# Kernel optimization log

Hardware: AMD Instinct MI355X
Metric: run time of the kernel (lower is better)

## Reference

```python
import jax, jax.numpy as jnp
import numpy as np

TWO_PI = 2.0 * np.pi
B, S_IN, S_OUT, K, HID = 1024, 4096, 4096, 8, 512
EPS = 1e-6


def setup_inputs() -> dict:
    key = jax.random.key(0)
    k1, k2, k3, k4, k5, k6, k7, k8 = jax.random.split(key, 8)
    x_in = jax.random.uniform(k1, (B, S_OUT), dtype=jnp.float32) * TWO_PI
    x_passive = jax.random.normal(k2, (B, S_IN), dtype=jnp.float32)
    log_density = jax.random.normal(k3, (B, 1), dtype=jnp.float32)
    # MLP params (nn.Linear default-ish init scale)
    lim1 = 1.0 / np.sqrt(S_IN)
    lim2 = 1.0 / np.sqrt(HID)
    w1 = jax.random.uniform(k4, (S_IN, HID), jnp.float32, -lim1, lim1)
    b1 = jax.random.uniform(k5, (HID,), jnp.float32, -lim1, lim1)
    w2 = jax.random.uniform(k6, (HID, S_OUT * 3 * K), jnp.float32, -lim2, lim2)
    b2 = jax.random.uniform(k7, (S_OUT * 3 * K,), jnp.float32, -lim2, lim2)
    phase_shift = jax.random.uniform(k8, (1,), jnp.float32)
    return {"x_in": x_in, "x_passive": x_passive, "log_density": log_density,
            "w1": w1, "b1": b1, "w2": w2, "b2": b2, "phase_shift": phase_shift}


def reference(x_in, x_passive, log_density, w1, b1, w2, b2, phase_shift):
    # normalise network input with global mean / (unbiased) std, as torch does
    xn = (x_passive - x_passive.mean()) / x_passive.std(ddof=1)
    # dense network: Linear -> tanh -> Linear -> tanh (final_activation=activation)
    net = jnp.tanh(jnp.tanh(xn @ w1 + b1) @ w2 + b2)            # (B, S*3K)
    net = net.reshape(-1, S_OUT, 3 * K)
    h_raw, w_raw, d_raw = net[..., :K], net[..., K:2 * K], net[..., 2 * K:]
    h_norm = jax.nn.softmax(h_raw, axis=2) * TWO_PI              # (B,S,K)
    w_norm = jax.nn.softmax(w_raw, axis=2) * TWO_PI
    d_norm = jax.nn.softplus(d_raw)
    bshape = (h_norm.shape[0], S_OUT, 1)
    x_kp = jnp.concatenate([jnp.full(bshape, -EPS, h_norm.dtype),
                            jnp.cumsum(w_norm, axis=2)], axis=2)  # (B,S,K+1)
    phi_kp = jnp.concatenate([jnp.zeros(bshape, h_norm.dtype),
                              jnp.cumsum(h_norm, axis=2)], axis=2)
    x = x_in[..., None]                                          # (B,S,1)
    # searchsorted (left) per element: count of knots strictly less than x, minus 1
    k_ind = jnp.sum(x_kp < x, axis=2, keepdims=True) - 1         # (B,S,1) int
    k_ind = jnp.clip(k_ind, 0, K - 1)
    g = lambda a, i: jnp.take_along_axis(a, i, axis=2)
    w_k = g(w_norm, k_ind)
    h_k = g(h_norm, k_ind)
    s_k = h_k / w_k
    d_k = g(d_norm, k_ind)
    d_kp1 = g(d_norm, (k_ind + 1) % K)
    x_km1 = g(x_kp, k_ind)
    phi_km1 = g(phi_kp, k_ind)
    alpha = (x - x_km1) / w_k
    a1m = alpha * (1.0 - alpha)
    denom = s_k + (d_kp1 + d_k - 2.0 * s_k) * a1m
    phi_out = (phi_km1 + h_k * (s_k * alpha ** 2 + d_k * a1m) / denom)[..., 0]
    phi_out = (phi_out + phase_shift) % TWO_PI                   # (B,S)
    grad = s_k ** 2 * (d_kp1 * alpha ** 2 + 2.0 * s_k * a1m
                       + d_k * (1.0 - alpha) ** 2) / denom ** 2  # (B,S,1)
    log_density = log_density - jnp.log(grad).sum(axis=1)        # (B,1)
    return phi_out, log_density
```

## Files before the change

kernel.cpp:

```cpp
#include <hip/hip_runtime.h>
#include <cstdint>
#include <cstddef>


typedef unsigned short u16;
typedef __bf16 bf16x8 __attribute__((ext_vector_type(8)));
typedef float f32x4 __attribute__((ext_vector_type(4)));
typedef unsigned short u16x8 __attribute__((ext_vector_type(8)));
typedef unsigned short u16x4 __attribute__((ext_vector_type(4)));
typedef unsigned short u16x2 __attribute__((ext_vector_type(2)));

#define TWOPI_F 6.28318530717958647692f

static __device__ __forceinline__ u16 f32_to_bf16(float f){
  unsigned u = __builtin_bit_cast(unsigned, f);
  return (u16)((u + 0x7fffu + ((u >> 16) & 1u)) >> 16);
}
static __device__ __forceinline__ void async16(void* lds, const void* g){
  __builtin_amdgcn_global_load_lds((const __attribute__((address_space(1))) void*)g,
                                   (__attribute__((address_space(3))) void*)lds,
                                   16, 0, 0);
}
static __device__ __forceinline__ float rcpf(float x){ return __builtin_amdgcn_rcpf(x); }
static __device__ __forceinline__ float fast_tanh(float x){
  x = fminf(fmaxf(x, -15.f), 15.f);
  float e = __expf(2.f * x);
  return (e - 1.f) / (e + 1.f);
}
static __device__ __forceinline__ float tanh_nc(float x){
  const float e2 = __expf(2.f * x);
  return 1.f - 2.f * rcpf(e2 + 1.f);
}
static __device__ __forceinline__ float exp_tanh(float x){
  const float e2 = __expf(2.f * x);
  const float u  = rcpf(e2 + 1.f);
  return __expf(1.f - 2.f * u);
}
static __device__ __forceinline__ float softplus_f(float x){
  return fmaxf(x, 0.f) + __logf(1.f + __expf(-fabsf(x)));
}

__global__ void k_stats(const float* __restrict__ xp, float* __restrict__ stats){
  __shared__ float ss[4], sq[4];
  const int tid = threadIdx.x;
  const long gt = (long)blockIdx.x * 256 + tid;
  const float4* x4 = (const float4*)xp;
  float s = 0.f, q = 0.f;
  #pragma unroll
  for (int p = 0; p < 4; ++p){
    float4 v = x4[gt + (long)p * 262144];
    s += v.x + v.y + v.z + v.w;
    q += v.x*v.x + v.y*v.y + v.z*v.z + v.w*v.w;
  }
  #pragma unroll
  for (int off = 32; off; off >>= 1){
    s += __shfl_down(s, off);
    q += __shfl_down(q, off);
  }
  if ((tid & 63) == 0){ ss[tid>>6] = s; sq[tid>>6] = q; }
  __syncthreads();
  if (tid == 0){
    atomicAdd(stats,     ss[0]+ss[1]+ss[2]+ss[3]);
    atomicAdd(stats + 1, sq[0]+sq[1]+sq[2]+sq[3]);
  }
}

__global__ void k_prep(const float* __restrict__ xp, const float* __restrict__ stats,
                       u16* __restrict__ xn){
  const long t = (long)blockIdx.x * 256 + threadIdx.x;
  const float sum = stats[0], sq = stats[1];
  const float N = 4194304.f;
  const float mean = sum / N;
  const float istd = rsqrtf((sq - sum*sum/N) / (N - 1.f));
  const float4* x4 = (const float4*)xp;
  const float4 a = x4[2*t], b = x4[2*t+1];
  u16x8 o;
  o[0]=f32_to_bf16((a.x-mean)*istd); o[1]=f32_to_bf16((a.y-mean)*istd);
  o[2]=f32_to_bf16((a.z-mean)*istd); o[3]=f32_to_bf16((a.w-mean)*istd);
  o[4]=f32_to_bf16((b.x-mean)*istd); o[5]=f32_to_bf16((b.y-mean)*istd);
  o[6]=f32_to_bf16((b.z-mean)*istd); o[7]=f32_to_bf16((b.w-mean)*istd);
  ((u16x8*)xn)[t] = o;
}

__global__ __launch_bounds__(256) void k_transpose_cvt(const float* __restrict__ in,
                                                       u16* __restrict__ out,
                                                       int Kd, int Nd){
  __shared__ __align__(16) u16 tT[128*256];
  const int tid = threadIdx.x;
  const long k0 = (long)blockIdx.x * 256, n0 = (long)blockIdx.y * 128;
  const int lam = tid & 31, g = tid >> 5;
  const int c = lam * 4;
  const int sig = (lam & 7) << 2;
  #pragma unroll
  for (int pass = 0; pass < 16; ++pass){
    const int P = pass*8 + g;
    const float4 f0 = *(const float4*)&in[(k0 + 2*P    )*Nd + n0 + c];
    const float4 f1 = *(const float4*)&in[(k0 + 2*P + 1)*Nd + n0 + c];
    const int pp = 2*(P ^ sig);
    *(u16x2*)&tT[(c    )*256 + pp] = u16x2{f32_to_bf16(f0.x), f32_to_bf16(f1.x)};
    *(u16x2*)&tT[(c + 1)*256 + pp] = u16x2{f32_to_bf16(f0.y), f32_to_bf16(f1.y)};
    *(u16x2*)&tT[(c + 2)*256 + pp] = u16x2{f32_to_bf16(f0.z), f32_to_bf16(f1.z)};
    *(u16x2*)&tT[(c + 3)*256 + pp] = u16x2{f32_to_bf16(f0.w), f32_to_bf16(f1.w)};
  }
  __syncthreads();
  const int w = tid >> 6, l = tid & 63;
  const int lh = l >> 5, lk = l & 31;
  #pragma unroll
  for (int it = 0; it < 16; ++it){
    const int n = (w << 5) + (it << 1) + lh;
    const int s2 = (n >> 2) & 7;
    const u16x8 v = *(const u16x8*)&tT[n*256 + 8*(lk ^ s2)];
    *(u16x8*)&out[(n0 + n)*Kd + k0 + 8*lk] = v;
  }
}

__global__ __launch_bounds__(256, 2) void k_gemm1(
    const u16* __restrict__ xn,
    const u16* __restrict__ w1t,
    float* __restrict__ pp)
{
  __shared__ __align__(16) u16 sA[4][64*32];
  __shared__ __align__(16) u16 sB[4][64*32];
  const int tid = threadIdx.x, lane = tid & 63, w = tid >> 6;
  const int n0 = blockIdx.x << 6, m0 = blockIdx.y << 6;
  const int ks = blockIdx.z;
  const int wm = w >> 1, wn = w & 1;
  const int rA = lane >> 2, cA = (lane & 3) << 3;
  const int fr = lane & 15, fq = lane >> 4;
  const f32x4 z4 = {0.f, 0.f, 0.f, 0.f};
  f32x4 acc[2][2];
  #pragma unroll
  for (int i=0;i<2;i++){ acc[i][0] = z4; acc[i][1] = z4; }

  auto stage = [&](int kt){
    const int b = kt & 3;
    const int kofs = (ks << 11) + (kt << 5) + cA;
    async16(sA[b] + w*512, xn  + (long)(m0 + w*16 + rA)*4096 + kofs);
    async16(sB[b] + w*512, w1t + (long)(n0 + w*16 + rA)*4096 + kofs);
  };

  stage(0); stage(1);
  for (int kt = 0; kt < 64; ++kt){
    if (kt < 62){
      stage(kt + 2);
      asm volatile("s_waitcnt vmcnt(4)" ::: "memory");
    } else if (kt == 62){
      asm volatile("s_waitcnt vmcnt(2)" ::: "memory");
    } else {
      asm volatile("s_waitcnt vmcnt(0)" ::: "memory");
    }
    __builtin_amdgcn_s_barrier();
    const int b = kt & 3;
    bf16x8 af[2], bfv[2];
    #pragma unroll
    for (int i=0;i<2;i++) af[i]  = *(const bf16x8*)(sA[b] + ((wm<<5) + i*16 + fr)*32 + (fq<<3));
    #pragma unroll
    for (int j=0;j<2;j++) bfv[j] = *(const bf16x8*)(sB[b] + ((wn<<5) + j*16 + fr)*32 + (fq<<3));
    #pragma unroll
    for (int i=0;i<2;i++)
      #pragma unroll
      for (int j=0;j<2;j++)
        acc[i][j] = __builtin_amdgcn_mfma_f32_16x16x32_bf16(af[i], bfv[j], acc[i][j], 0, 0, 0);
  }
  float* po = pp + ((size_t)ks << 19);
  #pragma unroll
  for (int i=0;i<2;i++)
    #pragma unroll
    for (int j=0;j<2;j++)
      #pragma unroll
      for (int r=0;r<4;r++){
        const int row = m0 + (wm<<5) + i*16 + (fq<<2) + r;
        const int col = n0 + (wn<<5) + j*16 + fr;
        po[row*512 + col] = acc[i][j][r];
      }
}

__global__ void k_gemm1b(const float* __restrict__ pp, const float* __restrict__ b1,
                         u16* __restrict__ hb){
  const int t = blockIdx.x * 256 + threadIdx.x;
  const float4 a = ((const float4*)pp)[t];
  const float4 b = ((const float4*)pp)[131072 + t];
  const float4 bb = ((const float4*)b1)[t & 127];
  u16x4 o;
  o[0] = f32_to_bf16(fast_tanh(a.x + b.x + bb.x));
  o[1] = f32_to_bf16(fast_tanh(a.y + b.y + bb.y));
  o[2] = f32_to_bf16(fast_tanh(a.z + b.z + bb.z));
  o[3] = f32_to_bf16(fast_tanh(a.w + b.w + bb.w));
  ((u16x4*)hb)[t] = o;
}

__global__ __launch_bounds__(256, 2) void k_gemm2(
    const u16* __restrict__ hmat,
    const u16* __restrict__ w2t,
    const float* __restrict__ b2,
    const float* __restrict__ x_in,
    const float* __restrict__ phase,
    float* __restrict__ phi_out,
    float* __restrict__ part)
{
  __shared__ __align__(16) char smem[25600];
  u16* sA = (u16*)smem;
  u16* sB = (u16*)(smem + 16384);
  float* sC = (float*)smem;

  const int tid  = threadIdx.x;
  const int lane = tid & 63;
  const int w    = tid >> 6;
  const int id   = blockIdx.x;
  const int work = ((id & 7) << 9) | (id >> 3);
  const int m0   = (work & 3) << 8;
  const int nt   = work >> 2;
  const long n0  = (long)nt * 96;

  const int rA = lane >> 2, cA = (lane & 3) << 3;
  const int fr = lane & 15, fq = lane >> 4;

  const f32x4 z4 = {0.f, 0.f, 0.f, 0.f};
  f32x4 acc[4][6];
  #pragma unroll
  for (int i=0;i<4;i++)
    #pragma unroll
    for (int j=0;j<6;j++) acc[i][j] = z4;

  #pragma unroll 4
  for (int kt = 0; kt < 16; ++kt){
    const int kofs = (kt << 5) + cA;
    #pragma unroll
    for (int cc = 0; cc < 4; ++cc){
      const int c = (w << 2) + cc;
      async16(sA + c*512, hmat + (long)(m0 + c*16 + rA)*512 + kofs);
    }
    #pragma unroll
    for (int cc = 0; cc < 2; ++cc){
      const int ch = (w << 1) + cc;
      int row = ch*16 + rA; if (row > 95) row = 95;
      async16(sB + ch*512, w2t + (n0 + row)*512 + kofs);
    }
    __syncthreads();
    bf16x8 af[4], bfv[6];
    #pragma unroll
    for (int i=0;i<4;i++)
      af[i] = *(const bf16x8*)(sA + ((w<<6) + i*16 + fr)*32 + (fq<<3));
    #pragma unroll
    for (int j=0;j<6;j++)
      bfv[j] = *(const bf16x8*)(sB + (j*16 + fr)*32 + (fq<<3));
    #pragma unroll
    for (int i=0;i<4;i++)
      #pragma unroll
      for (int j=0;j<6;j++)
        acc[i][j] = __builtin_amdgcn_mfma_f32_16x16x32_bf16(af[i], bfv[j], acc[i][j], 0, 0, 0);
    __syncthreads();
  }

  const float shift = phase[0];
  float b2c[6];
  #pragma unroll
  for (int j=0;j<6;j++) b2c[j] = b2[n0 + j*16 + fr];
  float* myC = sC + w*1600;

  #pragma unroll
  for (int q = 0; q < 4; ++q){
    #pragma unroll
    for (int j=0;j<6;j++)
      #pragma unroll
      for (int r=0;r<4;r++)
        myC[((fq<<2)+r)*100 + j*16 + fr] = acc[q][j][r] + b2c[j];

    const int row = fr;
    const int g   = fq;
    const float* tp = myC + row*100 + g*24;
    float t[16];
    #pragma unroll
    for (int jj=0;jj<4;jj++){
      const f32x4 v = *(const f32x4*)(tp + 4*jj);
      t[4*jj] = v[0]; t[4*jj+1] = v[1]; t[4*jj+2] = v[2]; t[4*jj+3] = v[3];
    }

    const int bg = m0 + (w<<6) + (q<<4) + row;
    const int s  = (nt<<2) + g;
    const float x = x_in[(long)bg*4096 + s];

    float eh[8], ew[8];
    float sh = 0.f, sw = 0.f;
    #pragma unroll
    for (int i=0;i<8;i++){ eh[i] = exp_tanh(t[i]);   sh += eh[i]; }
    #pragma unroll
    for (int i=0;i<8;i++){ ew[i] = exp_tanh(t[8+i]); sw += ew[i]; }

    const float xs = x * sw * (1.f / TWOPI_F);
    float cw = 0.f; int k = 0;
    #pragma unroll
    for (int i=0;i<8;i++){ cw += ew[i]; k += (cw < xs) ? 1 : 0; }
    if (k > 7) k = 7;

    float wkr = 0.f, hkr = 0.f, xkr = 0.f, phr = 0.f;
    float c2 = 0.f, h2 = 0.f;
    #pragma unroll
    for (int i=0;i<8;i++){
      if (i == k){ wkr = ew[i]; hkr = eh[i]; xkr = c2; phr = h2; }
      c2 += ew[i]; h2 += eh[i];
    }

    const float* dp = tp + 16;
    const float th0 = tanh_nc(dp[k]);
    const float th1 = tanh_nc(dp[(k + 1) & 7]);
    const float dk  = __logf(1.f + __expf(th0));
    const float dk1 = __logf(1.f + __expf(th1));

    const float rsh = rcpf(sh);
    const float rwk = rcpf(wkr);
    const float alpha = (xs - xkr) * rwk;
    const float sk = hkr * rwk * (sw * rsh);
    const float hk = TWOPI_F * hkr * rsh;
    const float ph = TWOPI_F * phr * rsh;
    const float a1m = alpha * (1.f - alpha);
    const float denom = sk + (dk1 + dk - 2.f*sk)*a1m;
    const float rd = rcpf(denom);
    const float phiv = ph + hk*(sk*alpha*alpha + dk*a1m)*rd;
    float p = phiv + shift;
    if (p >= TWOPI_F) p -= TWOPI_F;
    if (p >= TWOPI_F) p -= TWOPI_F;
    phi_out[(long)bg*4096 + s] = p;

    const float om = 1.f - alpha;
    const float num = dk1*alpha*alpha + 2.f*sk*a1m + dk*om*om;
    const float srd = sk * rd;
    float lg = __logf(srd*srd*num);
    lg += __shfl_xor(lg, 16);
    lg += __shfl_xor(lg, 32);
    if (lane < 16) part[(long)bg*1024 + nt] = lg;
  }
}

__global__ void k_ldred(const float* __restrict__ part, const float* __restrict__ ldin,
                        float* __restrict__ ldout){
  __shared__ float ss[4];
  const int b = blockIdx.x, tid = threadIdx.x;
  const float4* p4 = (const float4*)(part + ((long)b << 10));
  const float4 v = p4[tid];
  float s = v.x + v.y + v.z + v.w;
  #pragma unroll
  for (int off = 32; off; off >>= 1) s += __shfl_down(s, off);
  if ((tid & 63) == 0) ss[tid >> 6] = s;
  __syncthreads();
  if (tid == 0) ldout[b] = ldin[b] - (ss[0]+ss[1]+ss[2]+ss[3]);
}

extern "C" void kernel_launch(void* const* d_in, const int* in_sizes, int n_in,
                              void* d_out, int out_size, void* d_ws, size_t ws_size,
                              hipStream_t stream){
  (void)in_sizes; (void)n_in; (void)out_size; (void)ws_size;
  const float* x_in  = (const float*)d_in[0];
  const float* x_pas = (const float*)d_in[1];
  const float* ldin  = (const float*)d_in[2];
  const float* w1    = (const float*)d_in[3];
  const float* b1    = (const float*)d_in[4];
  const float* w2    = (const float*)d_in[5];
  const float* b2    = (const float*)d_in[6];
  const float* phase = (const float*)d_in[7];
  float* out   = (float*)d_out;
  float* phi   = out;
  float* ldout = out + (size_t)1024*4096;

  char* ws = (char*)d_ws;
  float* stats = (float*)ws;
  u16* xn   = (u16*)(ws + 256);
  u16* w1t  = (u16*)(ws + 8388864);
  u16* hb   = (u16*)(ws + 12583168);
  u16* w2t  = (u16*)(ws + 13631744);
  float* part = (float*)(ws + 114295040);

  hipMemsetAsync(stats, 0, 8, stream);
  k_stats<<<1024, 256, 0, stream>>>(x_pas, stats);
  k_prep<<<2048, 256, 0, stream>>>(x_pas, stats, xn);
  k_transpose_cvt<<<dim3(16, 4),  256, 0, stream>>>(w1, w1t, 4096, 512);
  k_transpose_cvt<<<dim3(2, 768), 256, 0, stream>>>(w2, w2t, 512, 98304);
  k_gemm1<<<dim3(8, 16, 2), 256, 0, stream>>>(xn, w1t, part);
  k_gemm1b<<<512, 256, 0, stream>>>(part, b1, hb);
  k_gemm2<<<dim3(4096), 256, 0, stream>>>(hb, w2t, b2, x_in, phase, phi, part);
  k_ldred<<<1024, 256, 0, stream>>>(part, ldin, ldout);
}
```

Before: 536.8 us.

## Pipeline GEMM2 K-loop with 4-slot LDS ring for B and direct A register loads

Restructures the second GEMM's K-loop so A fragments are loaded straight from global memory into double-buffered registers, skipping LDS. B tiles are staged asynchronously two iterations ahead into a four-slot LDS ring, synchronised with manual vmcnt waits and a single barrier per iteration. This replaces the two barriers per iteration and the load-then-compute serialisation. The cost is more registers, more LDS (32KB), and fragile hand-counted waitcnt values.

```diff
diff --git a/kernel.cpp b/kernel.cpp
--- a/kernel.cpp
+++ b/kernel.cpp
@@ -35,9 +35,6 @@
   const float e2 = __expf(2.f * x);
   const float u  = rcpf(e2 + 1.f);
   return __expf(1.f - 2.f * u);
-}
-static __device__ __forceinline__ float softplus_f(float x){
-  return fmaxf(x, 0.f) + __logf(1.f + __expf(-fabsf(x)));
 }
 
 __global__ void k_stats(const float* __restrict__ xp, float* __restrict__ stats){
@@ -198,10 +195,7 @@
     float* __restrict__ phi_out,
     float* __restrict__ part)
 {
-  __shared__ __align__(16) char smem[25600];
-  u16* sA = (u16*)smem;
-  u16* sB = (u16*)(smem + 16384);
-  float* sC = (float*)smem;
+  __shared__ __align__(16) char smem[32768];
 
   const int tid  = threadIdx.x;
   const int lane = tid & 63;
@@ -222,36 +216,49 @@
     #pragma unroll
     for (int j=0;j<6;j++) acc[i][j] = z4;
 
-  #pragma unroll 4
-  for (int kt = 0; kt < 16; ++kt){
+  const u16* aptr = hmat + (long)(m0 + (w<<6) + fr)*512 + (fq<<3);
+  bf16x8 af[2][4];
+
+  auto stageB = [&](int kt){
+    u16* slot = (u16*)(smem + ((kt & 3) << 13));
     const int kofs = (kt << 5) + cA;
-    #pragma unroll
-    for (int cc = 0; cc < 4; ++cc){
-      const int c = (w << 2) + cc;
-      async16(sA + c*512, hmat + (long)(m0 + c*16 + rA)*512 + kofs);
-    }
     #pragma unroll
     for (int cc = 0; cc < 2; ++cc){
       const int ch = (w << 1) + cc;
       int row = ch*16 + rA; if (row > 95) row = 95;
-      async16(sB + ch*512, w2t + (n0 + row)*512 + kofs);
+      async16(slot + ch*512, w2t + (n0 + row)*512 + kofs);
     }
-    __syncthreads();
-    bf16x8 af[4], bfv[6];
+  };
+  auto loadA = [&](int kt, int s){
     #pragma unroll
     for (int i=0;i<4;i++)
-      af[i] = *(const bf16x8*)(sA + ((w<<6) + i*16 + fr)*32 + (fq<<3));
+      af[s][i] = *(const bf16x8*)(aptr + ((long)i<<13) + (kt<<5));
+  };
+
+  stageB(0); stageB(1); loadA(0, 0);
+  #pragma unroll 2
+  for (int kt = 0; kt < 16; ++kt){
+    if (kt < 15) loadA(kt + 1, (kt + 1) & 1);
+    if (kt < 14) stageB(kt + 2);
+    if (kt == 0)       asm volatile("s_waitcnt vmcnt(6)" ::: "memory");
+    else if (kt <= 13) asm volatile("s_waitcnt vmcnt(8)" ::: "memory");
+    else if (kt == 14) asm volatile("s_waitcnt vmcnt(6)" ::: "memory");
+    else               asm volatile("s_waitcnt vmcnt(0)" ::: "memory");
+    __builtin_amdgcn_s_barrier();
+    const u16* bB = (const u16*)(smem + ((kt & 3) << 13));
+    bf16x8 bfv[6];
     #pragma unroll
     for (int j=0;j<6;j++)
-      bfv[j] = *(const bf16x8*)(sB + (j*16 + fr)*32 + (fq<<3));
+      bfv[j] = *(const bf16x8*)(bB + (j*16 + fr)*32 + (fq<<3));
     #pragma unroll
     for (int i=0;i<4;i++)
       #pragma unroll
       for (int j=0;j<6;j++)
-        acc[i][j] = __builtin_amdgcn_mfma_f32_16x16x32_bf16(af[i], bfv[j], acc[i][j], 0, 0, 0);
-    __syncthreads();
-  }
-
+        acc[i][j] = __builtin_amdgcn_mfma_f32_16x16x32_bf16(af[kt & 1][i], bfv[j], acc[i][j], 0, 0, 0);
+  }
+  __syncthreads();
+
+  float* sC = (float*)smem;
   const float shift = phase[0];
   float b2c[6];
   #pragma unroll
```

After: 575.0 us. 7.1% more time.
